# Optimization experiments

Measured on AMD Instinct MI355X. Metric: run time of the kernel, lower is better.

Reference implementation:

```python
import jax, jax.numpy as jnp
import numpy as np

EPS = 1e-7      # float32 eps from Hyperboloid.eps
MINN = 1e-15    # min_norm
MAXN = 1e6      # max_norm
# curvature c = 1 -> K = 1, sqrtK = 1

def _arcosh(x):
    xc = jnp.maximum(x, 1.0 + 1e-15)
    return jnp.log(jnp.maximum(xc + jnp.sqrt(xc * xc - 1.0), MINN))

def _cosh(x):
    return jnp.cosh(jnp.clip(x, -15.0, 15.0))

def _sinh(x):
    return jnp.sinh(jnp.clip(x, -15.0, 15.0))

def _mdot(x, y):  # Minkowski dot, keepdim
    return (jnp.sum(x * y, axis=-1) - 2.0 * x[..., 0] * y[..., 0])[..., None]

def _mnorm(u):
    return jnp.sqrt(jnp.maximum(_mdot(u, u), EPS))

def _proj(x):  # project onto hyperboloid by recomputing time coord
    y = x[:, 1:]
    first = jnp.sqrt(jnp.maximum(1.0 + jnp.sum(y * y, axis=-1, keepdims=True), EPS))
    return jnp.concatenate([first, y], axis=-1)

def _proj_tan(u, x):
    ux = jnp.sum(x[:, 1:] * u[:, 1:], axis=-1, keepdims=True)
    v0 = ux / jnp.maximum(x[:, 0:1], EPS)
    return jnp.concatenate([v0, u[:, 1:]], axis=-1)

def _expmap0(u):
    xr = u[:, 1:]
    xn = jnp.maximum(jnp.linalg.norm(xr, axis=-1, keepdims=True), MINN)
    return _proj(jnp.concatenate([_cosh(xn), _sinh(xn) * xr / xn], axis=-1))

def _logmap0(x):
    y = x[:, 1:]
    yn = jnp.maximum(jnp.linalg.norm(y, axis=-1, keepdims=True), MINN)
    theta = jnp.maximum(x[:, 0:1], 1.0 + EPS)
    return jnp.concatenate([jnp.zeros_like(theta), _arcosh(theta) * y / yn], axis=-1)

def _sqdist(x, y):
    theta = jnp.maximum(-_mdot(x, y), 1.0 + EPS)
    return jnp.minimum(_arcosh(theta) ** 2, 50.0)

def _logmap(x, y):
    xy = jnp.minimum(_mdot(x, y) + 1.0, -EPS) - 1.0
    u = y + xy * x
    nu = jnp.maximum(_mnorm(u), MINN)
    dist = jnp.sqrt(_sqdist(x, y))
    return _proj_tan(dist * u / nu, x)

def _expmap(u, x):
    theta = jnp.maximum(jnp.minimum(_mnorm(u), MAXN), MINN)
    return _proj(_cosh(theta) * x + _sinh(theta) * u / theta)

def _to_poincare(x):
    return x[:, 1:] / (x[:, 0:1] + 1.0)

def _to_hyperboloid(x):
    sq = jnp.sum(x * x, axis=-1, keepdims=True)
    return jnp.concatenate([1.0 + sq, 2.0 * x], axis=-1) / (1.0 - sq)

def _conv(x, src, dst, W, n):
    # message: mobius_matvec then logmap at target node
    out = _expmap0(_logmap0(x[src]) @ W.T)          # [E, D]
    msg = _logmap(out, x[dst])                      # [E, D]
    aggr = jax.ops.segment_sum(msg, dst, num_segments=n)  # scatter-add -> [N, D]
    # update: expmap at x, poincare relu, back to hyperboloid
    h = _expmap(aggr, x)
    p = jax.nn.relu(_to_poincare(h))
    return _to_hyperboloid(p)


def setup_inputs() -> dict:
    key = jax.random.key(0)
    ks = jax.random.split(key, 6)
    N, D, E = 50000, 128, 500000
    # valid hyperboloid points: expmap0 of a tangent vector at origin
    u = 0.1 * jax.random.normal(ks[0], (N, D), dtype=jnp.float32)
    x = _expmap0(u)
    edge_index = jax.random.randint(ks[1], (2, E), 0, N, dtype=jnp.int32)
    s = 1.0 / np.sqrt(D)
    W0 = s * jax.random.normal(ks[2], (D, D), dtype=jnp.float32)
    W1 = s * jax.random.normal(ks[3], (D, D), dtype=jnp.float32)
    Wf = s * jax.random.normal(ks[4], (D, D + 2 * D), dtype=jnp.float32)
    bf = 0.01 * jax.random.normal(ks[5], (D,), dtype=jnp.float32)
    return {"x": x, "edge_index": edge_index, "W0": W0, "W1": W1, "Wf": Wf, "bf": bf}


def reference(x, edge_index, W0, W1, Wf, bf):
    n = x.shape[0]
    src, dst = edge_index[0], edge_index[1]
    xs = [x]
    for W in (W0, W1):
        xs.append(_conv(xs[-1], src, dst, W, n))
    h = jnp.concatenate(xs, axis=-1)  # cat=True: [N, D + num_layers*D]
    return h @ Wf.T + bf              # final Linear
```

## Files before the change

### kernel.cpp

```cpp
#include <hip/hip_runtime.h>
#include <hip/hip_bf16.h>

#define EPSF  1e-7f
#define MINNF 1e-15f
#define BCAP  64

typedef __attribute__((ext_vector_type(8))) short short8v;
typedef __attribute__((ext_vector_type(8))) unsigned short ushort8v;
typedef __attribute__((ext_vector_type(4))) float f32x4;

__device__ __forceinline__ float wredsum(float v){
  #pragma unroll
  for (int m = 32; m; m >>= 1) v += __shfl_xor(v, m, 64);
  return v;
}

__device__ __forceinline__ float arcoshf_(float x){
  float xc = fmaxf(x, 1.0f);
  return __logf(fmaxf(xc + sqrtf(fmaxf(xc*xc - 1.0f, 0.0f)), MINNF));
}

__device__ __forceinline__ void sinhcosh_(float x, float& sh, float& ch){
  float xc = fminf(fmaxf(x, -15.0f), 15.0f);
  float e  = __expf(xc);
  float ei = 1.0f / e;
  ch = 0.5f * (e + ei);
  sh = 0.5f * (e - ei);
}

__device__ __forceinline__ short f2bf(float f){
  union { __hip_bfloat16 b; short s; } u;
  u.b = __float2bfloat16(f);
  return u.s;
}

__device__ __forceinline__ float bf2f(unsigned short u){
  union { unsigned int i; float f; } c;
  c.i = ((unsigned int)u) << 16;
  return c.f;
}

__device__ __forceinline__ short8v cvt8(float4 v0, float4 v1){
  short8v h;
  h[0]=f2bf(v0.x); h[1]=f2bf(v0.y); h[2]=f2bf(v0.z); h[3]=f2bf(v0.w);
  h[4]=f2bf(v1.x); h[5]=f2bf(v1.y); h[6]=f2bf(v1.z); h[7]=f2bf(v1.w);
  return h;
}

__global__ __launch_bounds__(256) void k_bucket(const int* __restrict__ src,
                                                const int* __restrict__ dst,
                                                int* __restrict__ deg,
                                                int* __restrict__ ssrc, int E,
                                                const float* __restrict__ X,
                                                float* __restrict__ Sv, int N){
  int gtid = blockIdx.x * 256 + threadIdx.x;
  if (gtid < E){
    int d = dst[gtid];
    int pos = atomicAdd(&deg[d], 1);
    if (pos < BCAP) ssrc[((size_t)d << 6) + pos] = src[gtid];
  }
  int w = gtid >> 6, lane = threadIdx.x & 63;
  int nw = (gridDim.x * 256) >> 6;
  for (int nd = w; nd < N; nd += nw){
    const float2 xv = *(const float2*)&X[(size_t)nd*128 + lane*2];
    float x0 = __shfl(xv.x, 0, 64);
    float ax = (lane == 0) ? 0.0f : xv.x;
    float yn2 = wredsum(ax*ax + xv.y*xv.y);
    float yn  = fmaxf(sqrtf(yn2), MINNF);
    float theta = fmaxf(x0, 1.0f + EPSF);
    if (lane == 0) Sv[nd] = arcoshf_(theta) / yn;
  }
}

__global__ __launch_bounds__(256) void k_conv(const unsigned short* __restrict__ OUT,
                                              const float* __restrict__ X,
                                              const int* __restrict__ deg,
                                              const int* __restrict__ ssrc,
                                              float* __restrict__ XN,
                                              float* __restrict__ Sout, int N){
  int node  = (blockIdx.x * blockDim.x + threadIdx.x) >> 6;
  int lane  = threadIdx.x & 63;
  int gbase = lane & 48;
  int l16   = lane & 15;
  if (node >= N) return;
  float x[8];
  {
    const float4 xlo = *(const float4*)&X[(size_t)node*128 + l16*8];
    const float4 xhi = *(const float4*)&X[(size_t)node*128 + l16*8 + 4];
    x[0]=xlo.x; x[1]=xlo.y; x[2]=xlo.z; x[3]=xlo.w;
    x[4]=xhi.x; x[5]=xhi.y; x[6]=xhi.z; x[7]=xhi.w;
  }
  float b0 = __shfl(x[0], gbase, 64);
  int beg = node << 6;
  int end = beg + min(deg[node], BCAP);
  float accA[8] = {0,0,0,0,0,0,0,0};
  float alpha = 0.f, acc0s = 0.f;

  int idx = beg + (gbase >> 4);
  bool okn = (idx < end);
  ushort8v araw = {0,0,0,0,0,0,0,0};
  if (okn) araw = *(const ushort8v*)&OUT[(size_t)ssrc[idx]*128 + l16*8];
  for (int it = beg; it < end; it += 4){
    ushort8v cur = araw;
    bool okc = okn;
    idx += 4; okn = (idx < end);
    if (okn) araw = *(const ushort8v*)&OUT[(size_t)ssrc[idx]*128 + l16*8];
    float a[8];
    #pragma unroll
    for (int j = 0; j < 8; ++j) a[j] = bf2f(cur[j]);
    float a0 = __shfl(a[0], gbase, 64);
    float dp = a[0]*x[0];
    #pragma unroll
    for (int j = 1; j < 8; ++j) dp = fmaf(a[j], x[j], dp);
    #pragma unroll
    for (int mm = 1; mm < 16; mm <<= 1) dp += __shfl_xor(dp, mm, 64);
    float m  = dp - 2.0f*a0*b0;
    float xy = fminf(m + 1.0f, -EPSF) - 1.0f;
    float m_uu = -1.0f + xy*(2.0f*m - xy);
    float nu = fmaxf(sqrtf(fmaxf(m_uu, EPSF)), MINNF);
    float th = fmaxf(-m, 1.0f + EPSF);
    float arc = arcoshf_(th);
    float dist = fminf(arc, 7.07106781f);
    float sc = __fdividef(dist, nu);
    float u0 = b0 + xy*a0;
    float v0 = sc*u0;
    float v0p = __fdividef(fmaf(sc, m - xy, a0*v0), fmaxf(a0, EPSF));
    float gam = okc ? sc*xy : 0.f;
    alpha += okc ? sc  : 0.f;
    acc0s += okc ? v0p : 0.f;
    #pragma unroll
    for (int j = 0; j < 8; ++j) accA[j] = fmaf(gam, a[j], accA[j]);
  }
  #pragma unroll
  for (int j = 0; j < 8; ++j){
    accA[j] += __shfl_xor(accA[j], 16, 64);
    accA[j] += __shfl_xor(accA[j], 32, 64);
  }
  alpha += __shfl_xor(alpha, 16, 64); alpha += __shfl_xor(alpha, 32, 64);
  acc0s += __shfl_xor(acc0s, 16, 64); acc0s += __shfl_xor(acc0s, 32, 64);

  float acc[8];
  #pragma unroll
  for (int j = 0; j < 8; ++j) acc[j] = fmaf(alpha, x[j], accA[j]);
  if (l16 == 0) acc[0] = acc0s;
  float u0 = acc0s;

  float md = 0.f;
  #pragma unroll
  for (int j = 0; j < 8; ++j) md = fmaf(acc[j], acc[j], md);
  #pragma unroll
  for (int mm = 1; mm < 16; mm <<= 1) md += __shfl_xor(md, mm, 64);
  md -= 2.0f*u0*u0;
  float theta = fmaxf(fminf(sqrtf(fmaxf(md, EPSF)), 1e6f), MINNF);
  float sh, ch; sinhcosh_(theta, sh, ch);
  float s = __fdividef(sh, theta);
  float h[8];
  #pragma unroll
  for (int j = 0; j < 8; ++j) h[j] = ch*x[j] + s*acc[j];
  if (l16 == 0) h[0] = 0.f;
  float hh = 0.f;
  #pragma unroll
  for (int j = 0; j < 8; ++j) hh = fmaf(h[j], h[j], hh);
  #pragma unroll
  for (int mm = 1; mm < 16; mm <<= 1) hh += __shfl_xor(hh, mm, 64);
  float h0 = sqrtf(fmaxf(1.0f + hh, EPSF));
  float inv = 1.0f / (h0 + 1.0f);
  float p[8];
  #pragma unroll
  for (int j = 0; j < 8; ++j) p[j] = fmaxf(h[j]*inv, 0.f);
  float sq = 0.f;
  #pragma unroll
  for (int j = 0; j < 8; ++j) sq = fmaf(p[j], p[j], sq);
  #pragma unroll
  for (int mm = 1; mm < 16; mm <<= 1) sq += __shfl_xor(sq, mm, 64);
  float idn = 1.0f / (1.0f - sq);
  float o[8];
  #pragma unroll
  for (int j = 0; j < 8; ++j) o[j] = 2.0f*p[j]*idn;
  if (l16 == 0) o[0] = (1.0f + sq)*idn;
  if (gbase == 0){
    float4 lo = make_float4(o[0], o[1], o[2], o[3]);
    float4 hi = make_float4(o[4], o[5], o[6], o[7]);
    *(float4*)&XN[(size_t)node*128 + l16*8]     = lo;
    *(float4*)&XN[(size_t)node*128 + l16*8 + 4] = hi;
  }
  if (Sout && lane == 0){
    float o0n  = (1.0f + sq)*idn;
    float ynrm = fmaxf(2.0f*idn*sqrtf(sq), MINNF);
    Sout[node] = arcoshf_(fmaxf(o0n, 1.0f + EPSF)) / ynrm;
  }
}

template<int DO_EXP>
__global__ __launch_bounds__(256) void gemm_mfma(const float* __restrict__ A0,
                                                 const float* __restrict__ A1,
                                                 const float* __restrict__ A2,
                                                 const float* __restrict__ W,
                                                 const float* __restrict__ bias,
                                                 const float* __restrict__ S,
                                                 float* __restrict__ Cf,
                                                 unsigned short* __restrict__ Cb,
                                                 int N, int nchunk){
  __shared__ __align__(16) char smraw[64*130*4];
  short* Asm = (short*)smraw;
  short* Wsm = Asm + 64*64;
  float* Csm = (float*)smraw;
  int tid  = threadIdx.x;
  int lane = tid & 63;
  int wid  = tid >> 6;
  int wr   = wid >> 1;
  int wc   = wid & 1;
  int base = blockIdx.x * 64;
  int ldw  = nchunk * 128;
  int nkt  = nchunk * 2;

  const f32x4 z4 = {0.f, 0.f, 0.f, 0.f};
  f32x4 acc[2][4];
  #pragma unroll
  for (int mi = 0; mi < 2; ++mi)
    #pragma unroll
    for (int ni = 0; ni < 4; ++ni) acc[mi][ni] = z4;

  for (int kt = 0; kt < nkt; ++kt){
    int ch = kt >> 1;
    const float* Ac = (ch == 0) ? A0 : ((ch == 1) ? A1 : A2);
    int cko = (kt & 1) * 64;
    #pragma unroll
    for (int t = 0; t < 2; ++t){
      int g = tid + t*256;
      int r = g >> 3;
      int kc = (g & 7) * 8;
      int nd = base + r;
      short8v h = {0,0,0,0,0,0,0,0};
      if (nd < N){
        const float* ap = &Ac[(size_t)nd*128 + cko + kc];
        float4 v0 = *(const float4*)ap;
        float4 v1 = *(const float4*)(ap + 4);
        if (S){
          float sn = S[nd];
          if (cko == 0 && kc == 0) v0.x = 0.0f;
          v0.x*=sn; v0.y*=sn; v0.z*=sn; v0.w*=sn;
          v1.x*=sn; v1.y*=sn; v1.z*=sn; v1.w*=sn;
        }
        h = cvt8(v0, v1);
      }
      int byte = (r*128 + kc*2) ^ ((r & 7) << 4);
      *(short8v*)((char*)Asm + byte) = h;
    }
    #pragma unroll
    for (int t = 0; t < 4; ++t){
      int g = tid + t*256;
      int j = g >> 3;
      int kc = (g & 7) * 8;
      const float* wp = &W[(size_t)j*ldw + kt*64 + kc];
      float4 v0 = *(const float4*)wp;
      float4 v1 = *(const float4*)(wp + 4);
      short8v h = cvt8(v0, v1);
      int byte = (j*128 + kc*2) ^ ((j & 7) << 4);
      *(short8v*)((char*)Wsm + byte) = h;
    }
    __syncthreads();
    #pragma unroll
    for (int ks = 0; ks < 2; ++ks){
      int kb = ks*64 + (lane >> 4) * 16;
      short8v af[2], bfv[4];
      #pragma unroll
      for (int mi = 0; mi < 2; ++mi){
        int r = wr*32 + mi*16 + (lane & 15);
        af[mi] = *(const short8v*)((const char*)Asm + ((r*128 + kb) ^ ((r & 7) << 4)));
      }
      #pragma unroll
      for (int ni = 0; ni < 4; ++ni){
        int j = wc*64 + ni*16 + (lane & 15);
        bfv[ni] = *(const short8v*)((const char*)Wsm + ((j*128 + kb) ^ ((j & 7) << 4)));
      }
      #pragma unroll
      for (int mi = 0; mi < 2; ++mi)
        #pragma unroll
        for (int ni = 0; ni < 4; ++ni)
          acc[mi][ni] = __builtin_amdgcn_mfma_f32_16x16x32_bf16(af[mi], bfv[ni], acc[mi][ni], 0, 0, 0);
    }
    __syncthreads();
  }

  if (DO_EXP){
    #pragma unroll
    for (int mi = 0; mi < 2; ++mi)
      #pragma unroll
      for (int rg = 0; rg < 4; ++rg){
        int r = wr*32 + mi*16 + (lane >> 4)*4 + rg;
        #pragma unroll
        for (int ni = 0; ni < 4; ++ni){
          int col = wc*64 + ni*16 + (lane & 15);
          Csm[r*130 + col] = acc[mi][ni][rg];
        }
      }
    __syncthreads();
    for (int rr = 0; rr < 16; ++rr){
      int r = wid*16 + rr;
      int nd = base + r;
      if (nd >= N) continue;
      float2 zv = *(const float2*)&Csm[r*130 + lane*2];
      float zx = (lane == 0) ? 0.0f : zv.x;
      float xn2 = wredsum(zx*zx + zv.y*zv.y);
      float xn  = fmaxf(sqrtf(xn2), MINNF);
      float sh, chh; sinhcosh_(xn, sh, chh);
      float s = sh / xn;
      float ox = s * zx;
      float oy = s * zv.y;
      float s2 = wredsum(ox*ox + oy*oy);
      float o0 = sqrtf(fmaxf(1.0f + s2, EPSF));
      if (lane == 0) ox = o0;
      unsigned int lo = (unsigned int)(unsigned short)f2bf(ox);
      unsigned int hi = (unsigned int)(unsigned short)f2bf(oy);
      *(unsigned int*)&Cb[(size_t)nd*128 + lane*2] = (hi << 16) | lo;
    }
  } else {
    #pragma unroll
    for (int mi = 0; mi < 2; ++mi){
      #pragma unroll
      for (int rg = 0; rg < 4; ++rg){
        int row = base + wr*32 + mi*16 + (lane >> 4)*4 + rg;
        if (row < N){
          #pragma unroll
          for (int ni = 0; ni < 4; ++ni){
            int col = wc*64 + ni*16 + (lane & 15);
            float v = acc[mi][ni][rg];
            if (bias) v += bias[col];
            Cf[(size_t)row*128 + col] = v;
          }
        }
      }
    }
  }
}

extern "C" void kernel_launch(void* const* d_in, const int* in_sizes, int n_in,
                              void* d_out, int out_size, void* d_ws, size_t ws_size,
                              hipStream_t stream) {
  const float* x0 = (const float*)d_in[0];
  const int*   ei = (const int*)  d_in[1];
  const float* W0 = (const float*)d_in[2];
  const float* W1 = (const float*)d_in[3];
  const float* Wf = (const float*)d_in[4];
  const float* bf = (const float*)d_in[5];
  float* out = (float*)d_out;

  int N = in_sizes[0] / 128;
  int E = in_sizes[1] / 2;
  const int* src = ei;
  const int* dst = ei + E;

  size_t row = (size_t)N * 128;
  float* ws = (float*)d_ws;
  float* x1 = ws;
  float* x2 = ws + row;
  float* Sv = ws + 2*row;
  size_t goff = ((2*row + (size_t)N) + 3) & ~(size_t)3;
  unsigned short* g16 = (unsigned short*)(ws + goff);
  int* deg  = (int*)(g16 + row);
  int* ssrc = deg + N;

  dim3 blk(256);
  int nodeBlocks = (N + 3) / 4;
  int eBlocks    = (E + 255) / 256;
  int gemmBlocks = (N + 63) / 64;

  hipMemsetAsync(deg, 0, (size_t)N * sizeof(int), stream);
  k_bucket<<<eBlocks, blk, 0, stream>>>(src, dst, deg, ssrc, E, x0, Sv, N);

  gemm_mfma<1> <<<gemmBlocks, blk, 0, stream>>>(x0, nullptr, nullptr, W0, nullptr, Sv, nullptr, g16, N, 1);
  k_conv       <<<nodeBlocks, blk, 0, stream>>>(g16, x0, deg, ssrc, x1, Sv, N);

  gemm_mfma<1> <<<gemmBlocks, blk, 0, stream>>>(x1, nullptr, nullptr, W1, nullptr, Sv, nullptr, g16, N, 1);
  k_conv       <<<nodeBlocks, blk, 0, stream>>>(g16, x1, deg, ssrc, x2, nullptr, N);

  gemm_mfma<0> <<<gemmBlocks, blk, 0, stream>>>(x0, x1, x2, Wf, bf, nullptr, out, nullptr, N, 3);
}
```

Before: 242.7 us.

## Make conv kernel persistent with next-node prefetch and store x2 as bf16

The conv kernel becomes a grid-stride persistent kernel with a fixed grid of 2048 blocks. Each wave prefetches the next node's degree and feature row while it processes the current node, which hides load latency. The second conv layer now writes its output in bf16, and the final GEMM reads that chunk directly as bf16 without a float-to-bf16 conversion. This halves the x2 write and read traffic, at the cost of holding x2 in bf16. That loss should not matter because the GEMM already converted its inputs to bf16.

```diff
diff --git a/kernel.cpp b/kernel.cpp
--- a/kernel.cpp
+++ b/kernel.cpp
@@ -72,135 +72,160 @@
   }
 }
 
+template<int OBF>
 __global__ __launch_bounds__(256) void k_conv(const unsigned short* __restrict__ OUT,
                                               const float* __restrict__ X,
                                               const int* __restrict__ deg,
                                               const int* __restrict__ ssrc,
-                                              float* __restrict__ XN,
+                                              void* __restrict__ XNv,
                                               float* __restrict__ Sout, int N){
-  int node  = (blockIdx.x * blockDim.x + threadIdx.x) >> 6;
+  int wgid  = (blockIdx.x * blockDim.x + threadIdx.x) >> 6;
+  int nwv   = (gridDim.x * blockDim.x) >> 6;
   int lane  = threadIdx.x & 63;
   int gbase = lane & 48;
   int l16   = lane & 15;
-  if (node >= N) return;
-  float x[8];
-  {
-    const float4 xlo = *(const float4*)&X[(size_t)node*128 + l16*8];
-    const float4 xhi = *(const float4*)&X[(size_t)node*128 + l16*8 + 4];
-    x[0]=xlo.x; x[1]=xlo.y; x[2]=xlo.z; x[3]=xlo.w;
-    x[4]=xhi.x; x[5]=xhi.y; x[6]=xhi.z; x[7]=xhi.w;
-  }
-  float b0 = __shfl(x[0], gbase, 64);
-  int beg = node << 6;
-  int end = beg + min(deg[node], BCAP);
-  float accA[8] = {0,0,0,0,0,0,0,0};
-  float alpha = 0.f, acc0s = 0.f;
-
-  int idx = beg + (gbase >> 4);
-  bool okn = (idx < end);
-  ushort8v araw = {0,0,0,0,0,0,0,0};
-  if (okn) araw = *(const ushort8v*)&OUT[(size_t)ssrc[idx]*128 + l16*8];
-  for (int it = beg; it < end; it += 4){
-    ushort8v cur = araw;
-    bool okc = okn;
-    idx += 4; okn = (idx < end);
+  float* XNf = (float*)XNv;
+  unsigned short* XNb = (unsigned short*)XNv;
+
+  int node = wgid;
+  int dcur = 0;
+  float4 rlo = make_float4(0,0,0,0), rhi = make_float4(0,0,0,0);
+  if (node < N){
+    dcur = min(deg[node], BCAP);
+    rlo = *(const float4*)&X[(size_t)node*128 + l16*8];
+    rhi = *(const float4*)&X[(size_t)node*128 + l16*8 + 4];
+  }
+
+  while (node < N){
+    float x[8];
+    x[0]=rlo.x; x[1]=rlo.y; x[2]=rlo.z; x[3]=rlo.w;
+    x[4]=rhi.x; x[5]=rhi.y; x[6]=rhi.z; x[7]=rhi.w;
+    int dc = dcur;
+    int nnode = node + nwv;
+    if (nnode < N){
+      dcur = min(deg[nnode], BCAP);
+      rlo = *(const float4*)&X[(size_t)nnode*128 + l16*8];
+      rhi = *(const float4*)&X[(size_t)nnode*128 + l16*8 + 4];
+    }
+
+    float b0 = __shfl(x[0], gbase, 64);
+    int beg = node << 6;
+    int end = beg + dc;
+    float accA[8] = {0,0,0,0,0,0,0,0};
+    float alpha = 0.f, acc0s = 0.f;
+
+    int idx = beg + (gbase >> 4);
+    bool okn = (idx < end);
+    ushort8v araw = {0,0,0,0,0,0,0,0};
     if (okn) araw = *(const ushort8v*)&OUT[(size_t)ssrc[idx]*128 + l16*8];
-    float a[8];
-    #pragma unroll
-    for (int j = 0; j < 8; ++j) a[j] = bf2f(cur[j]);
-    float a0 = __shfl(a[0], gbase, 64);
-    float dp = a[0]*x[0];
-    #pragma unroll
-    for (int j = 1; j < 8; ++j) dp = fmaf(a[j], x[j], dp);
-    #pragma unroll
-    for (int mm = 1; mm < 16; mm <<= 1) dp += __shfl_xor(dp, mm, 64);
-    float m  = dp - 2.0f*a0*b0;
-    float xy = fminf(m + 1.0f, -EPSF) - 1.0f;
-    float m_uu = -1.0f + xy*(2.0f*m - xy);
-    float nu = fmaxf(sqrtf(fmaxf(m_uu, EPSF)), MINNF);
-    float th = fmaxf(-m, 1.0f + EPSF);
-    float arc = arcoshf_(th);
-    float dist = fminf(arc, 7.07106781f);
-    float sc = __fdividef(dist, nu);
-    float u0 = b0 + xy*a0;
-    float v0 = sc*u0;
-    float v0p = __fdividef(fmaf(sc, m - xy, a0*v0), fmaxf(a0, EPSF));
-    float gam = okc ? sc*xy : 0.f;
-    alpha += okc ? sc  : 0.f;
-    acc0s += okc ? v0p : 0.f;
-    #pragma unroll
-    for (int j = 0; j < 8; ++j) accA[j] = fmaf(gam, a[j], accA[j]);
-  }
-  #pragma unroll
-  for (int j = 0; j < 8; ++j){
-    accA[j] += __shfl_xor(accA[j], 16, 64);
-    accA[j] += __shfl_xor(accA[j], 32, 64);
-  }
-  alpha += __shfl_xor(alpha, 16, 64); alpha += __shfl_xor(alpha, 32, 64);
-  acc0s += __shfl_xor(acc0s, 16, 64); acc0s += __shfl_xor(acc0s, 32, 64);
-
-  float acc[8];
-  #pragma unroll
-  for (int j = 0; j < 8; ++j) acc[j] = fmaf(alpha, x[j], accA[j]);
-  if (l16 == 0) acc[0] = acc0s;
-  float u0 = acc0s;
-
-  float md = 0.f;
-  #pragma unroll
-  for (int j = 0; j < 8; ++j) md = fmaf(acc[j], acc[j], md);
-  #pragma unroll
-  for (int mm = 1; mm < 16; mm <<= 1) md += __shfl_xor(md, mm, 64);
-  md -= 2.0f*u0*u0;
-  float theta = fmaxf(fminf(sqrtf(fmaxf(md, EPSF)), 1e6f), MINNF);
-  float sh, ch; sinhcosh_(theta, sh, ch);
-  float s = __fdividef(sh, theta);
-  float h[8];
-  #pragma unroll
-  for (int j = 0; j < 8; ++j) h[j] = ch*x[j] + s*acc[j];
-  if (l16 == 0) h[0] = 0.f;
-  float hh = 0.f;
-  #pragma unroll
-  for (int j = 0; j < 8; ++j) hh = fmaf(h[j], h[j], hh);
-  #pragma unroll
-  for (int mm = 1; mm < 16; mm <<= 1) hh += __shfl_xor(hh, mm, 64);
-  float h0 = sqrtf(fmaxf(1.0f + hh, EPSF));
-  float inv = 1.0f / (h0 + 1.0f);
-  float p[8];
-  #pragma unroll
-  for (int j = 0; j < 8; ++j) p[j] = fmaxf(h[j]*inv, 0.f);
-  float sq = 0.f;
-  #pragma unroll
-  for (int j = 0; j < 8; ++j) sq = fmaf(p[j], p[j], sq);
-  #pragma unroll
-  for (int mm = 1; mm < 16; mm <<= 1) sq += __shfl_xor(sq, mm, 64);
-  float idn = 1.0f / (1.0f - sq);
-  float o[8];
-  #pragma unroll
-  for (int j = 0; j < 8; ++j) o[j] = 2.0f*p[j]*idn;
-  if (l16 == 0) o[0] = (1.0f + sq)*idn;
-  if (gbase == 0){
-    float4 lo = make_float4(o[0], o[1], o[2], o[3]);
-    float4 hi = make_float4(o[4], o[5], o[6], o[7]);
-    *(float4*)&XN[(size_t)node*128 + l16*8]     = lo;
-    *(float4*)&XN[(size_t)node*128 + l16*8 + 4] = hi;
-  }
-  if (Sout && lane == 0){
-    float o0n  = (1.0f + sq)*idn;
-    float ynrm = fmaxf(2.0f*idn*sqrtf(sq), MINNF);
-    Sout[node] = arcoshf_(fmaxf(o0n, 1.0f + EPSF)) / ynrm;
+    for (int it = beg; it < end; it += 4){
+      ushort8v cur = araw;
+      bool okc = okn;
+      idx += 4; okn = (idx < end);
+      if (okn) araw = *(const ushort8v*)&OUT[(size_t)ssrc[idx]*128 + l16*8];
+      float a[8];
+      #pragma unroll
+      for (int j = 0; j < 8; ++j) a[j] = bf2f(cur[j]);
+      float a0 = __shfl(a[0], gbase, 64);
+      float dp = a[0]*x[0];
+      #pragma unroll
+      for (int j = 1; j < 8; ++j) dp = fmaf(a[j], x[j], dp);
+      #pragma unroll
+      for (int mm = 1; mm < 16; mm <<= 1) dp += __shfl_xor(dp, mm, 64);
+      float m  = dp - 2.0f*a0*b0;
+      float xy = fminf(m + 1.0f, -EPSF) - 1.0f;
+      float m_uu = -1.0f + xy*(2.0f*m - xy);
+      float nu = fmaxf(sqrtf(fmaxf(m_uu, EPSF)), MINNF);
+      float th = fmaxf(-m, 1.0f + EPSF);
+      float arc = arcoshf_(th);
+      float dist = fminf(arc, 7.07106781f);
+      float sc = __fdividef(dist, nu);
+      float u0 = b0 + xy*a0;
+      float v0 = sc*u0;
+      float v0p = __fdividef(fmaf(sc, m - xy, a0*v0), fmaxf(a0, EPSF));
+      float gam = okc ? sc*xy : 0.f;
+      alpha += okc ? sc  : 0.f;
+      acc0s += okc ? v0p : 0.f;
+      #pragma unroll
+      for (int j = 0; j < 8; ++j) accA[j] = fmaf(gam, a[j], accA[j]);
+    }
+    #pragma unroll
+    for (int j = 0; j < 8; ++j){
+      accA[j] += __shfl_xor(accA[j], 16, 64);
+      accA[j] += __shfl_xor(accA[j], 32, 64);
+    }
+    alpha += __shfl_xor(alpha, 16, 64); alpha += __shfl_xor(alpha, 32, 64);
+    acc0s += __shfl_xor(acc0s, 16, 64); acc0s += __shfl_xor(acc0s, 32, 64);
+
+    float acc[8];
+    #pragma unroll
+    for (int j = 0; j < 8; ++j) acc[j] = fmaf(alpha, x[j], accA[j]);
+    if (l16 == 0) acc[0] = acc0s;
+    float u0 = acc0s;
+
+    float md = 0.f;
+    #pragma unroll
+    for (int j = 0; j < 8; ++j) md = fmaf(acc[j], acc[j], md);
+    #pragma unroll
+    for (int mm = 1; mm < 16; mm <<= 1) md += __shfl_xor(md, mm, 64);
+    md -= 2.0f*u0*u0;
+    float theta = fmaxf(fminf(sqrtf(fmaxf(md, EPSF)), 1e6f), MINNF);
+    float sh, ch; sinhcosh_(theta, sh, ch);
+    float s = __fdividef(sh, theta);
+    float h[8];
+    #pragma unroll
+    for (int j = 0; j < 8; ++j) h[j] = ch*x[j] + s*acc[j];
+    if (l16 == 0) h[0] = 0.f;
+    float hh = 0.f;
+    #pragma unroll
+    for (int j = 0; j < 8; ++j) hh = fmaf(h[j], h[j], hh);
+    #pragma unroll
+    for (int mm = 1; mm < 16; mm <<= 1) hh += __shfl_xor(hh, mm, 64);
+    float h0 = sqrtf(fmaxf(1.0f + hh, EPSF));
+    float inv = 1.0f / (h0 + 1.0f);
+    float p[8];
+    #pragma unroll
+    for (int j = 0; j < 8; ++j) p[j] = fmaxf(h[j]*inv, 0.f);
+    float sq = 0.f;
+    #pragma unroll
+    for (int j = 0; j < 8; ++j) sq = fmaf(p[j], p[j], sq);
+    #pragma unroll
+    for (int mm = 1; mm < 16; mm <<= 1) sq += __shfl_xor(sq, mm, 64);
+    float idn = 1.0f / (1.0f - sq);
+    float o[8];
+    #pragma unroll
+    for (int j = 0; j < 8; ++j) o[j] = 2.0f*p[j]*idn;
+    if (l16 == 0) o[0] = (1.0f + sq)*idn;
+    if (gbase == 0){
+      if (OBF){
+        ushort8v ov;
+        #pragma unroll
+        for (int j = 0; j < 8; ++j) ov[j] = (unsigned short)f2bf(o[j]);
+        *(ushort8v*)&XNb[(size_t)node*128 + l16*8] = ov;
+      } else {
+        *(float4*)&XNf[(size_t)node*128 + l16*8]     = make_float4(o[0], o[1], o[2], o[3]);
+        *(float4*)&XNf[(size_t)node*128 + l16*8 + 4] = make_float4(o[4], o[5], o[6], o[7]);
+      }
+    }
+    if (Sout && lane == 0){
+      float o0n  = (1.0f + sq)*idn;
+      float ynrm = fmaxf(2.0f*idn*sqrtf(sq), MINNF);
+      Sout[node] = arcoshf_(fmaxf(o0n, 1.0f + EPSF)) / ynrm;
+    }
+    node = nnode;
   }
 }
 
 template<int DO_EXP>
-__global__ __launch_bounds__(256) void gemm_mfma(const float* __restrict__ A0,
-                                                 const float* __restrict__ A1,
-                                                 const float* __restrict__ A2,
+__global__ __launch_bounds__(256) void gemm_mfma(const void* __restrict__ A0,
+                                                 const void* __restrict__ A1,
+                                                 const void* __restrict__ A2,
                                                  const float* __restrict__ W,
                                                  const float* __restrict__ bias,
                                                  const float* __restrict__ S,
                                                  float* __restrict__ Cf,
                                                  unsigned short* __restrict__ Cb,
-                                                 int N, int nchunk){
+                                                 int N, int nchunk, int abf){
   __shared__ __align__(16) char smraw[64*130*4];
   short* Asm = (short*)smraw;
   short* Wsm = Asm + 64*64;
@@ -223,7 +248,8 @@
 
   for (int kt = 0; kt < nkt; ++kt){
     int ch = kt >> 1;
-    const float* Ac = (ch == 0) ? A0 : ((ch == 1) ? A1 : A2);
+    const void* Ac = (ch == 0) ? A0 : ((ch == 1) ? A1 : A2);
+    bool isbf = (abf >> ch) & 1;
     int cko = (kt & 1) * 64;
     #pragma unroll
     for (int t = 0; t < 2; ++t){
@@ -233,16 +259,22 @@
       int nd = base + r;
       short8v h = {0,0,0,0,0,0,0,0};
       if (nd < N){
-        const float* ap = &Ac[(size_t)nd*128 + cko + kc];
-        float4 v0 = *(const float4*)ap;
-        float4 v1 = *(const float4*)(ap + 4);
-        if (S){
-          float sn = S[nd];
-          if (cko == 0 && kc == 0) v0.x = 0.0f;
-          v0.x*=sn; v0.y*=sn; v0.z*=sn; v0.w*=sn;
-          v1.x*=sn; v1.y*=sn; v1.z*=sn; v1.w*=sn;
+        if (isbf){
+          ushort8v raw = *(const ushort8v*)((const unsigned short*)Ac + (size_t)nd*128 + cko + kc);
+          #pragma unroll
+          for (int j = 0; j < 8; ++j) h[j] = (short)raw[j];
+        } else {
+          const float* ap = (const float*)Ac + (size_t)nd*128 + cko + kc;
+          float4 v0 = *(const float4*)ap;
+          float4 v1 = *(const float4*)(ap + 4);
+          if (S){
+            float sn = S[nd];
+            if (cko == 0 && kc == 0) v0.x = 0.0f;
+            v0.x*=sn; v0.y*=sn; v0.z*=sn; v0.w*=sn;
+            v1.x*=sn; v1.y*=sn; v1.z*=sn; v1.w*=sn;
+          }
+          h = cvt8(v0, v1);
         }
-        h = cvt8(v0, v1);
       }
       int byte = (r*128 + kc*2) ^ ((r & 7) << 4);
       *(short8v*)((char*)Asm + byte) = h;
@@ -352,28 +384,30 @@
   const int* dst = ei + E;
 
   size_t row = (size_t)N * 128;
-  float* ws = (float*)d_ws;
-  float* x1 = ws;
-  float* x2 = ws + row;
-  float* Sv = ws + 2*row;
-  size_t goff = ((2*row + (size_t)N) + 3) & ~(size_t)3;
-  unsigned short* g16 = (unsigned short*)(ws + goff);
-  int* deg  = (int*)(g16 + row);
-  int* ssrc = deg + N;
+  char* ws = (char*)d_ws;
+  float* x1 = (float*)ws;
+  unsigned short* x2b = (unsigned short*)(x1 + row);
+  unsigned short* g16 = x2b + row;
+  float* Sv  = (float*)(g16 + row);
+  int* deg   = (int*)(Sv + N);
+  int* ssrc  = deg + N;
 
   dim3 blk(256);
-  int nodeBlocks = (N + 3) / 4;
   int eBlocks    = (E + 255) / 256;
   int gemmBlocks = (N + 63) / 64;
+  int convBlocks = 2048;
 
   hipMemsetAsync(deg, 0, (size_t)N * sizeof(int), stream);
   k_bucket<<<eBlocks, blk, 0, stream>>>(src, dst, deg, ssrc, E, x0, Sv, N);
 
-  gemm_mfma<1> <<<gemmBlocks, blk, 0, stream>>>(x0, nullptr, nullptr, W0, nullptr, Sv, nullptr, g16, N, 1);
-  k_conv       <<<nodeBlocks, blk, 0, stream>>>(g16, x0, deg, ssrc, x1, Sv, N);
-
-  gemm_mfma<1> <<<gemmBlocks, blk, 0, stream>>>(x1, nullptr, nullptr, W1, nullptr, Sv, nullptr, g16, N, 1);
-  k_conv       <<<nodeBlocks, blk, 0, stream>>>(g16, x1, deg, ssrc, x2, nullptr, N);
-
-  gemm_mfma<0> <<<gemmBlocks, blk, 0, stream>>>(x0, x1, x2, Wf, bf, nullptr, out, nullptr, N, 3);
-}
+  gemm_mfma<1><<<gemmBlocks, blk, 0, stream>>>(x0, nullptr, nullptr, W0, nullptr, Sv,
+                                               nullptr, g16, N, 1, 0);
+  k_conv<0>   <<<convBlocks, blk, 0, stream>>>(g16, x0, deg, ssrc, x1, Sv, N);
+
+  gemm_mfma<1><<<gemmBlocks, blk, 0, stream>>>(x1, nullptr, nullptr, W1, nullptr, Sv,
+                                               nullptr, g16, N, 1, 0);
+  k_conv<1>   <<<convBlocks, blk, 0, stream>>>(g16, x1, deg, ssrc, x2b, nullptr, N);
+
+  gemm_mfma<0><<<gemmBlocks, blk, 0, stream>>>(x0, x1, x2b, Wf, bf, nullptr,
+                                               out, nullptr, N, 3, 0b100);
+}
```

Result: slower. 267.3 us (+10.2%).
